# Performance work log

Measured on AMD Instinct MI355X. Metric: run time of the kernel, lower is better.

Reference implementation:

```python
import jax, jax.numpy as jnp
import numpy as np

N = 50000
D = 64
E = 800000


def setup_inputs() -> dict:
    key = jax.random.key(0)
    ks = jax.random.split(key, 8)
    x = jax.random.normal(ks[0], (N, D), dtype=jnp.float32)
    edge_index = jax.random.randint(ks[1], (2, E), 0, N, dtype=jnp.int64)
    edge_attr = jax.random.normal(ks[2], (E,), dtype=jnp.float32)
    x_agg_emb = jax.random.normal(ks[3], (N, D), dtype=jnp.float32)
    # Linear(2D -> D) weights stored as [in, out]; scale ~ kaiming-ish
    W_msg = jax.random.normal(ks[4], (2 * D, D), dtype=jnp.float32) * (1.0 / np.sqrt(2 * D))
    b_msg = jnp.zeros((D,), dtype=jnp.float32)
    W_upd = jax.random.normal(ks[5], (2 * D, D), dtype=jnp.float32) * (1.0 / np.sqrt(2 * D))
    b_upd = jnp.zeros((D,), dtype=jnp.float32)
    return {"x": x, "edge_index": edge_index, "edge_attr": edge_attr,
            "x_agg_emb": x_agg_emb, "W_msg": W_msg, "b_msg": b_msg,
            "W_upd": W_upd, "b_upd": b_upd}


def reference(x, edge_index, edge_attr, x_agg_emb, W_msg, b_msg, W_upd, b_upd):
    col, row = edge_index[0], edge_index[1]
    # edge-weighted gather: [E, D]
    msgs = edge_attr[:, None] * x[col]
    # scatter-mean over destination nodes (dim_size = N)
    summed = jax.ops.segment_sum(msgs, row, num_segments=N)            # [N, D]
    counts = jax.ops.segment_sum(jnp.ones_like(edge_attr), row, num_segments=N)  # [N]
    x_agg = summed / jnp.maximum(counts, 1.0)[:, None]
    # message MLP: Linear(2D->D) + ReLU
    m = jax.nn.relu(jnp.concatenate([x_agg, x_agg_emb], axis=-1) @ W_msg + b_msg)
    # update MLP: Linear(2D->D) + ReLU
    out = jax.nn.relu(jnp.concatenate([x, m], axis=-1) @ W_upd + b_upd)
    return out
```

## Files before the change

### kernel.cpp

```cpp
#include <hip/hip_runtime.h>


#define CAP 64
#define FILLB 2048

typedef __attribute__((ext_vector_type(8))) short short8;
typedef __attribute__((ext_vector_type(4))) float f32x4;

__device__ __forceinline__ unsigned short f2bf(float f) {
    unsigned int u = __float_as_uint(f);
    u += 0x7FFFu + ((u >> 16) & 1u);
    return (unsigned short)(u >> 16);
}
__device__ __forceinline__ uint4 pack8(const float* v) {
    uint4 r;
    r.x = (unsigned)f2bf(v[0]) | ((unsigned)f2bf(v[1]) << 16);
    r.y = (unsigned)f2bf(v[2]) | ((unsigned)f2bf(v[3]) << 16);
    r.z = (unsigned)f2bf(v[4]) | ((unsigned)f2bf(v[5]) << 16);
    r.w = (unsigned)f2bf(v[6]) | ((unsigned)f2bf(v[7]) << 16);
    return r;
}

__global__ __launch_bounds__(256) void zero_f32(float* p, int n) {
    int i = blockIdx.x * 256 + threadIdx.x;
    if (i < n) p[i] = 0.0f;
}
__global__ __launch_bounds__(256) void zero_i32(int* p, int n) {
    int i = blockIdx.x * 256 + threadIdx.x;
    if (i < n) p[i] = 0;
}

__global__ __launch_bounds__(256) void fill_group_kernel(
    const int* __restrict__ ei, const float* __restrict__ ea,
    int* cnt, int2* __restrict__ packed, int E, int N)
{
    const int g   = blockIdx.x & 7;
    const int bg  = blockIdx.x >> 3;
    const int nb  = gridDim.x >> 3;
    const int rpg = (N + 7) >> 3;
    const int rlo = g * rpg;
    const int rhi = min(rlo + rpg, N);
    const int chunk = (E + nb - 1) / nb;
    const int lo = bg * chunk;
    const int hi = min(lo + chunk, E);
    for (int e = lo + (int)threadIdx.x; e < hi; e += 256) {
        int row = ei[E + e];
        if (row >= rlo && row < rhi) {
            int pos = atomicAdd(&cnt[row], 1);
            if (pos < CAP)
                packed[(size_t)row * CAP + pos] =
                    make_int2(ei[e], __float_as_int(ea[e]));
        }
    }
}

__global__ __launch_bounds__(256) void gather_cap_kernel(
    const int2* __restrict__ packed, const int* __restrict__ cnt,
    const float* __restrict__ x, float* __restrict__ out, int N)
{
    const int g   = blockIdx.x & 7;
    const int i   = blockIdx.x >> 3;
    const int rpg = (N + 7) >> 3;
    const int nlo = g * rpg;
    int n = nlo + i * 4 + ((int)threadIdx.x >> 6);
    if (n >= nlo + rpg || n >= N) return;
    int lane = threadIdx.x & 63;
    const int2* seg = packed + (size_t)n * CAP;
    int deg = cnt[n];
    int dl = min(deg, CAP);
    float a0 = 0.f, a1 = 0.f, a2 = 0.f, a3 = 0.f;
    int j = 0;
    for (; j + 4 <= dl; j += 4) {
        int4 q0 = ((const int4*)seg)[(j >> 1)];
        int4 q1 = ((const int4*)seg)[(j >> 1) + 1];
        a0 += __int_as_float(q0.y) * x[(size_t)q0.x * 64 + lane];
        a1 += __int_as_float(q0.w) * x[(size_t)q0.z * 64 + lane];
        a2 += __int_as_float(q1.y) * x[(size_t)q1.x * 64 + lane];
        a3 += __int_as_float(q1.w) * x[(size_t)q1.z * 64 + lane];
    }
    for (; j < dl; j++) {
        int2 p = seg[j];
        a0 += __int_as_float(p.y) * x[(size_t)p.x * 64 + lane];
    }
    float acc = (a0 + a1) + (a2 + a3);
    out[(size_t)n * 64 + lane] = acc / fmaxf((float)deg, 1.0f);
}


__global__ __launch_bounds__(256) void hist_kernel(
    const int* __restrict__ ei, int* hist, int E)
{
    int e = blockIdx.x * 256 + threadIdx.x;
    if (e < E) atomicAdd(&hist[ei[E + e]], 1);
}
__global__ __launch_bounds__(256) void scan_partial_kernel(
    const int* __restrict__ hist, int* partial, int N)
{
    __shared__ int s[256];
    int t = threadIdx.x;
    int i = blockIdx.x * 256 + t;
    s[t] = (i < N) ? hist[i] : 0;
    __syncthreads();
    #pragma unroll
    for (int off = 128; off > 0; off >>= 1) {
        if (t < off) s[t] += s[t + off];
        __syncthreads();
    }
    if (t == 0) partial[blockIdx.x] = s[0];
}
__global__ __launch_bounds__(256) void scan_top_kernel(
    const int* __restrict__ partial, int* scanP, int NB)
{
    __shared__ int s[256];
    int t = threadIdx.x;
    int v = (t < NB) ? partial[t] : 0;
    s[t] = v;
    __syncthreads();
    #pragma unroll
    for (int off = 1; off < 256; off <<= 1) {
        int add = (t >= off) ? s[t - off] : 0;
        __syncthreads();
        s[t] += add;
        __syncthreads();
    }
    if (t < NB) scanP[t] = s[t] - v;
}
__global__ __launch_bounds__(256) void scan_final_kernel(
    const int* __restrict__ hist, const int* __restrict__ scanP,
    int* offsets, int* cursor, int N)
{
    __shared__ int s[256];
    int t = threadIdx.x;
    int i = blockIdx.x * 256 + t;
    int v = (i < N) ? hist[i] : 0;
    s[t] = v;
    __syncthreads();
    #pragma unroll
    for (int off = 1; off < 256; off <<= 1) {
        int add = (t >= off) ? s[t - off] : 0;
        __syncthreads();
        s[t] += add;
        __syncthreads();
    }
    if (i < N) {
        int o = scanP[blockIdx.x] + s[t] - v;
        offsets[i] = o;
        cursor[i]  = o;
    }
}
__global__ __launch_bounds__(256) void fill_kernel(
    const int* __restrict__ ei, const float* __restrict__ ea,
    int* cursor, int2* __restrict__ packed, int E)
{
    int e = blockIdx.x * 256 + threadIdx.x;
    if (e >= E) return;
    int pos = atomicAdd(&cursor[ei[E + e]], 1);
    packed[pos] = make_int2(ei[e], __float_as_int(ea[e]));
}
__global__ __launch_bounds__(256) void gather_kernel(
    const int2* __restrict__ packed, const int* __restrict__ offsets,
    const int* __restrict__ hist, const float* __restrict__ x,
    float* __restrict__ out, int N)
{
    int t = threadIdx.x;
    int n = blockIdx.x * 4 + (t >> 6);
    int lane = t & 63;
    if (n >= N) return;
    int start = offsets[n];
    int deg   = hist[n];
    float a0 = 0.f, a1 = 0.f, a2 = 0.f, a3 = 0.f;
    int j = 0;
    for (; j + 4 <= deg; j += 4) {
        int2 p0 = packed[start + j];
        int2 p1 = packed[start + j + 1];
        int2 p2 = packed[start + j + 2];
        int2 p3 = packed[start + j + 3];
        a0 += __int_as_float(p0.y) * x[(size_t)p0.x * 64 + lane];
        a1 += __int_as_float(p1.y) * x[(size_t)p1.x * 64 + lane];
        a2 += __int_as_float(p2.y) * x[(size_t)p2.x * 64 + lane];
        a3 += __int_as_float(p3.y) * x[(size_t)p3.x * 64 + lane];
    }
    for (; j < deg; j++) {
        int2 p = packed[start + j];
        a0 += __int_as_float(p.y) * x[(size_t)p.x * 64 + lane];
    }
    float acc = (a0 + a1) + (a2 + a3);
    out[(size_t)n * 64 + lane] = acc / fmaxf((float)deg, 1.0f);
}


__global__ __launch_bounds__(256) void scatter_kernel(
    const int* __restrict__ ei, const float* __restrict__ ea,
    const float* __restrict__ x, float* summed, float* counts, int E)
{
    int idx = blockIdx.x * 256 + threadIdx.x;
    int e = idx >> 6;
    int d = idx & 63;
    if (e >= E) return;
    float v = ea[e] * x[(size_t)ei[e] * 64 + d];
    atomicAdd(&summed[(size_t)ei[E + e] * 64 + d], v);
    if (d == 0) atomicAdd(&counts[ei[E + e]], 1.0f);
}


__device__ __forceinline__ void stage_W(
    unsigned short* Wb, const float* Wg, int t)
{
    #pragma unroll
    for (int c = t; c < 1024; c += 256) {
        int R = c >> 6, nn = c & 63;
        int kt = R >> 2, qq = R & 3;
        const float* src = Wg + (size_t)(kt * 32 + qq * 8) * 64 + nn;
        float v[8];
        #pragma unroll
        for (int j = 0; j < 8; j++) v[j] = src[(size_t)j * 64];
        *(uint4*)&Wb[R * 528 + nn * 8] = pack8(v);
    }
}

__device__ __forceinline__ void mfma_tile(
    const unsigned short* Ab, const unsigned short* Wb,
    int wv, int lane, f32x4 acc[4])
{
    const int q  = lane >> 4;
    const int ln = lane & 15;
    const int rr = wv * 16 + ln;
    short8 af[4];
    #pragma unroll
    for (int kt = 0; kt < 4; kt++)
        af[kt] = *(const short8*)&Ab[rr * 128 + (((kt * 4 + q) ^ ln) * 8)];
    #pragma unroll
    for (int nt = 0; nt < 4; nt++) {
        #pragma unroll
        for (int kt = 0; kt < 4; kt++) {
            short8 bf = *(const short8*)&Wb[(kt * 4 + q) * 528 + (nt * 16 + ln) * 8];
            acc[nt] = __builtin_amdgcn_mfma_f32_16x16x32_bf16(af[kt], bf, acc[nt], 0, 0, 0);
        }
    }
}

__global__ __launch_bounds__(256) void mfma_mlp(
    const float* Aagg, const float* __restrict__ Aemb,
    const float* __restrict__ counts, const float* __restrict__ Xin,
    const float* __restrict__ Wm, const float* __restrict__ bm,
    const float* __restrict__ Wu, const float* __restrict__ bu,
    float* out, int N)
{
    __shared__ __align__(16) unsigned short Ab[64 * 128];
    __shared__ __align__(16) unsigned short Wb[16 * 528];

    const int t = threadIdx.x;
    const int tile0 = blockIdx.x * 64;
    const int lane = t & 63, wv = t >> 6;
    const int q = lane >> 4, ln = lane & 15;

    stage_W(Wb, Wm, t);
    #pragma unroll
    for (int s = t; s < 1024; s += 256) {
        int r = s >> 4, chunk = s & 15;
        int node = tile0 + r;
        float v[8] = {0.f, 0.f, 0.f, 0.f, 0.f, 0.f, 0.f, 0.f};
        if (node < N) {
            const float* src = (chunk < 8)
                ? (Aagg + (size_t)node * 64 + chunk * 8)
                : (Aemb + (size_t)node * 64 + (chunk - 8) * 8);
            float4 p0 = ((const float4*)src)[0];
            float4 p1 = ((const float4*)src)[1];
            v[0] = p0.x; v[1] = p0.y; v[2] = p0.z; v[3] = p0.w;
            v[4] = p1.x; v[5] = p1.y; v[6] = p1.z; v[7] = p1.w;
            if (counts && chunk < 8) {
                float rc = 1.0f / fmaxf(counts[node], 1.0f);
                #pragma unroll
                for (int i = 0; i < 8; i++) v[i] *= rc;
            }
        }
        *(uint4*)&Ab[r * 128 + ((chunk ^ (r & 15)) * 8)] = pack8(v);
    }
    __syncthreads();

    f32x4 acc[4];
    #pragma unroll
    for (int nt = 0; nt < 4; nt++) acc[nt] = (f32x4){0.f, 0.f, 0.f, 0.f};
    mfma_tile(Ab, Wb, wv, lane, acc);
    __syncthreads();

    stage_W(Wb, Wu, t);
    #pragma unroll
    for (int s = t; s < 512; s += 256) {
        int r = s >> 3, chunk = s & 7;
        int node = tile0 + r;
        float v[8] = {0.f, 0.f, 0.f, 0.f, 0.f, 0.f, 0.f, 0.f};
        if (node < N) {
            const float* src = Xin + (size_t)node * 64 + chunk * 8;
            float4 p0 = ((const float4*)src)[0];
            float4 p1 = ((const float4*)src)[1];
            v[0] = p0.x; v[1] = p0.y; v[2] = p0.z; v[3] = p0.w;
            v[4] = p1.x; v[5] = p1.y; v[6] = p1.z; v[7] = p1.w;
        }
        *(uint4*)&Ab[r * 128 + ((chunk ^ (r & 15)) * 8)] = pack8(v);
    }
    #pragma unroll
    for (int nt = 0; nt < 4; nt++) {
        float bmv = bm[nt * 16 + ln];
        #pragma unroll
        for (int reg = 0; reg < 4; reg++) {
            float mv = fmaxf(acc[nt][reg] + bmv, 0.f);
            int rr = wv * 16 + q * 4 + reg;
            int k  = 64 + nt * 16 + ln;
            int ch = k >> 3;
            Ab[rr * 128 + ((ch ^ (rr & 15)) * 8) + (k & 7)] = f2bf(mv);
        }
    }
    __syncthreads();

    f32x4 acc2[4];
    #pragma unroll
    for (int nt = 0; nt < 4; nt++) acc2[nt] = (f32x4){0.f, 0.f, 0.f, 0.f};
    mfma_tile(Ab, Wb, wv, lane, acc2);
    #pragma unroll
    for (int nt = 0; nt < 4; nt++) {
        float buv = bu[nt * 16 + ln];
        #pragma unroll
        for (int reg = 0; reg < 4; reg++) {
            int rr = wv * 16 + q * 4 + reg;
            int node = tile0 + rr;
            if (node < N)
                out[(size_t)node * 64 + nt * 16 + ln] =
                    fmaxf(acc2[nt][reg] + buv, 0.f);
        }
    }
}

extern "C" void kernel_launch(void* const* d_in, const int* in_sizes, int n_in,
                              void* d_out, int out_size, void* d_ws, size_t ws_size,
                              hipStream_t stream) {
    const float* x   = (const float*)d_in[0];
    const int*   ei  = (const int*)d_in[1];
    const float* ea  = (const float*)d_in[2];
    const float* emb = (const float*)d_in[3];
    const float* Wm  = (const float*)d_in[4];
    const float* bm  = (const float*)d_in[5];
    const float* Wu  = (const float*)d_in[6];
    const float* bu  = (const float*)d_in[7];
    float*       out = (float*)d_out;

    const int N = in_sizes[0] / 64;
    const int E = in_sizes[2];
    const int NB = (N + 255) / 256;

    const int eblocks = (E + 255) / 256;
    const int mblocks = (N + 63) / 64;
    const int rpg = (N + 7) / 8;

    const size_t need_cap = (size_t)N * CAP * 8 + (size_t)N * 4;
    const size_t need_csr = (size_t)E * 8 + ((size_t)3 * N + 512) * 4;

    if (ws_size >= need_cap) {
        char* ws = (char*)d_ws;
        int2* packed = (int2*)ws;
        int*  cnt    = (int*)(ws + (size_t)N * CAP * 8);

        zero_i32<<<NB, 256, 0, stream>>>(cnt, N);
        fill_group_kernel<<<FILLB, 256, 0, stream>>>(ei, ea, cnt, packed, E, N);
        int gblocks = 8 * ((rpg + 3) / 4);
        gather_cap_kernel<<<gblocks, 256, 0, stream>>>(packed, cnt, x, out, N);
        mfma_mlp<<<mblocks, 256, 0, stream>>>(out, emb, nullptr, x,
                                              Wm, bm, Wu, bu, out, N);
    } else if (ws_size >= need_csr && NB <= 256) {
        char* ws = (char*)d_ws;
        int2* packed  = (int2*)ws;
        int*  hist    = (int*)(ws + (size_t)E * 8);
        int*  offsets = hist + N;
        int*  cursor  = offsets + N;
        int*  partial = cursor + N;
        int*  scanP   = partial + 256;

        zero_i32<<<NB, 256, 0, stream>>>(hist, N);
        hist_kernel<<<eblocks, 256, 0, stream>>>(ei, hist, E);
        scan_partial_kernel<<<NB, 256, 0, stream>>>(hist, partial, N);
        scan_top_kernel<<<1, 256, 0, stream>>>(partial, scanP, NB);
        scan_final_kernel<<<NB, 256, 0, stream>>>(hist, scanP, offsets, cursor, N);
        fill_kernel<<<eblocks, 256, 0, stream>>>(ei, ea, cursor, packed, E);
        gather_kernel<<<(N + 3) / 4, 256, 0, stream>>>(packed, offsets, hist, x, out, N);
        mfma_mlp<<<mblocks, 256, 0, stream>>>(out, emb, nullptr, x,
                                              Wm, bm, Wu, bu, out, N);
    } else {
        float* counts = (float*)d_ws;
        zero_f32<<<(N * 64 + 255) / 256, 256, 0, stream>>>(out, N * 64);
        zero_f32<<<NB, 256, 0, stream>>>(counts, N);
        long long total = (long long)E * 64;
        scatter_kernel<<<(int)((total + 255) / 256), 256, 0, stream>>>(
            ei, ea, x, out, counts, E);
        mfma_mlp<<<mblocks, 256, 0, stream>>>(out, emb, counts, x,
                                              Wm, bm, Wu, bu, out, N);
    }
}
```

Baseline: 174.5 us.

## Convert node features to bf16 upfront and gather/MLP on bf16 buffers

Adds a prep kernel that converts x and x_agg_emb to bf16 once and also zeroes the degree counters, replacing the separate zero kernel. The gather then reads bf16 rows of x and writes a bf16 aggregate, and a new MLP kernel loads bf16 tiles straight into shared memory without converting them. This halves the bytes moved by the random-access gather and by the MLP loads. In exchange it adds an extra pass over x and emb and extra workspace, and x is rounded to bf16 before aggregation, which changes numerics slightly.

```diff
diff --git a/kernel.cpp b/kernel.cpp
--- a/kernel.cpp
+++ b/kernel.cpp
@@ -11,6 +11,9 @@
     unsigned int u = __float_as_uint(f);
     u += 0x7FFFu + ((u >> 16) & 1u);
     return (unsigned short)(u >> 16);
+}
+__device__ __forceinline__ float bf2f(unsigned short u) {
+    return __uint_as_float((unsigned int)u << 16);
 }
 __device__ __forceinline__ uint4 pack8(const float* v) {
     uint4 r;
@@ -28,6 +31,29 @@
 __global__ __launch_bounds__(256) void zero_i32(int* p, int n) {
     int i = blockIdx.x * 256 + threadIdx.x;
     if (i < n) p[i] = 0;
+}
+
+__global__ __launch_bounds__(256) void prep_kernel(
+    const float* __restrict__ x, const float* __restrict__ emb,
+    unsigned short* __restrict__ xb, unsigned short* __restrict__ eb,
+    int* __restrict__ cnt, int N)
+{
+    int i = blockIdx.x * 256 + threadIdx.x;
+    int base = i * 8;
+    if (base < N * 64) {
+        float v[8];
+        float4 p0 = ((const float4*)(x + base))[0];
+        float4 p1 = ((const float4*)(x + base))[1];
+        v[0]=p0.x; v[1]=p0.y; v[2]=p0.z; v[3]=p0.w;
+        v[4]=p1.x; v[5]=p1.y; v[6]=p1.z; v[7]=p1.w;
+        *(uint4*)(xb + base) = pack8(v);
+        p0 = ((const float4*)(emb + base))[0];
+        p1 = ((const float4*)(emb + base))[1];
+        v[0]=p0.x; v[1]=p0.y; v[2]=p0.z; v[3]=p0.w;
+        v[4]=p1.x; v[5]=p1.y; v[6]=p1.z; v[7]=p1.w;
+        *(uint4*)(eb + base) = pack8(v);
+    }
+    if (i < N) cnt[i] = 0;
 }
 
 __global__ __launch_bounds__(256) void fill_group_kernel(
@@ -54,9 +80,10 @@
     }
 }
 
-__global__ __launch_bounds__(256) void gather_cap_kernel(
+__global__ __launch_bounds__(256) void gather_bf_kernel(
     const int2* __restrict__ packed, const int* __restrict__ cnt,
-    const float* __restrict__ x, float* __restrict__ out, int N)
+    const unsigned short* __restrict__ xb,
+    unsigned short* __restrict__ aggb, int N)
 {
     const int g   = blockIdx.x & 7;
     const int i   = blockIdx.x >> 3;
@@ -73,17 +100,17 @@
     for (; j + 4 <= dl; j += 4) {
         int4 q0 = ((const int4*)seg)[(j >> 1)];
         int4 q1 = ((const int4*)seg)[(j >> 1) + 1];
-        a0 += __int_as_float(q0.y) * x[(size_t)q0.x * 64 + lane];
-        a1 += __int_as_float(q0.w) * x[(size_t)q0.z * 64 + lane];
-        a2 += __int_as_float(q1.y) * x[(size_t)q1.x * 64 + lane];
-        a3 += __int_as_float(q1.w) * x[(size_t)q1.z * 64 + lane];
+        a0 += __int_as_float(q0.y) * bf2f(xb[(size_t)q0.x * 64 + lane]);
+        a1 += __int_as_float(q0.w) * bf2f(xb[(size_t)q0.z * 64 + lane]);
+        a2 += __int_as_float(q1.y) * bf2f(xb[(size_t)q1.x * 64 + lane]);
+        a3 += __int_as_float(q1.w) * bf2f(xb[(size_t)q1.z * 64 + lane]);
     }
     for (; j < dl; j++) {
         int2 p = seg[j];
-        a0 += __int_as_float(p.y) * x[(size_t)p.x * 64 + lane];
+        a0 += __int_as_float(p.y) * bf2f(xb[(size_t)p.x * 64 + lane]);
     }
     float acc = (a0 + a1) + (a2 + a3);
-    out[(size_t)n * 64 + lane] = acc / fmaxf((float)deg, 1.0f);
+    aggb[(size_t)n * 64 + lane] = f2bf(acc / fmaxf((float)deg, 1.0f));
 }
 
 
@@ -239,6 +266,84 @@
     }
 }
 
+__global__ __launch_bounds__(256) void mfma_mlp_bf(
+    const unsigned short* __restrict__ aggb, const unsigned short* __restrict__ eb,
+    const unsigned short* __restrict__ xb,
+    const float* __restrict__ Wm, const float* __restrict__ bm,
+    const float* __restrict__ Wu, const float* __restrict__ bu,
+    float* __restrict__ out, int N)
+{
+    __shared__ __align__(16) unsigned short Ab[64 * 128];
+    __shared__ __align__(16) unsigned short Wb[16 * 528];
+
+    const int t = threadIdx.x;
+    const int tile0 = blockIdx.x * 64;
+    const int lane = t & 63, wv = t >> 6;
+    const int q = lane >> 4, ln = lane & 15;
+
+    stage_W(Wb, Wm, t);
+    #pragma unroll
+    for (int s = t; s < 1024; s += 256) {
+        int r = s >> 4, chunk = s & 15;
+        int node = tile0 + r;
+        uint4 v = make_uint4(0u, 0u, 0u, 0u);
+        if (node < N) {
+            const unsigned short* src = (chunk < 8)
+                ? (aggb + (size_t)node * 64 + chunk * 8)
+                : (eb   + (size_t)node * 64 + (chunk - 8) * 8);
+            v = *(const uint4*)src;
+        }
+        *(uint4*)&Ab[r * 128 + ((chunk ^ (r & 15)) * 8)] = v;
+    }
+    __syncthreads();
+
+    f32x4 acc[4];
+    #pragma unroll
+    for (int nt = 0; nt < 4; nt++) acc[nt] = (f32x4){0.f, 0.f, 0.f, 0.f};
+    mfma_tile(Ab, Wb, wv, lane, acc);
+    __syncthreads();
+
+    stage_W(Wb, Wu, t);
+    #pragma unroll
+    for (int s = t; s < 512; s += 256) {
+        int r = s >> 3, chunk = s & 7;
+        int node = tile0 + r;
+        uint4 v = make_uint4(0u, 0u, 0u, 0u);
+        if (node < N) v = *(const uint4*)(xb + (size_t)node * 64 + chunk * 8);
+        *(uint4*)&Ab[r * 128 + ((chunk ^ (r & 15)) * 8)] = v;
+    }
+    #pragma unroll
+    for (int nt = 0; nt < 4; nt++) {
+        float bmv = bm[nt * 16 + ln];
+        #pragma unroll
+        for (int reg = 0; reg < 4; reg++) {
+            float mv = fmaxf(acc[nt][reg] + bmv, 0.f);
+            int rr = wv * 16 + q * 4 + reg;
+            int k  = 64 + nt * 16 + ln;
+            int ch = k >> 3;
+            Ab[rr * 128 + ((ch ^ (rr & 15)) * 8) + (k & 7)] = f2bf(mv);
+        }
+    }
+    __syncthreads();
+
+    f32x4 acc2[4];
+    #pragma unroll
+    for (int nt = 0; nt < 4; nt++) acc2[nt] = (f32x4){0.f, 0.f, 0.f, 0.f};
+    mfma_tile(Ab, Wb, wv, lane, acc2);
+    #pragma unroll
+    for (int nt = 0; nt < 4; nt++) {
+        float buv = bu[nt * 16 + ln];
+        #pragma unroll
+        for (int reg = 0; reg < 4; reg++) {
+            int rr = wv * 16 + q * 4 + reg;
+            int node = tile0 + rr;
+            if (node < N)
+                out[(size_t)node * 64 + nt * 16 + ln] =
+                    fmaxf(acc2[nt][reg] + buv, 0.f);
+        }
+    }
+}
+
 __global__ __launch_bounds__(256) void mfma_mlp(
     const float* Aagg, const float* __restrict__ Aemb,
     const float* __restrict__ counts, const float* __restrict__ Xin,
@@ -266,8 +371,8 @@
                 : (Aemb + (size_t)node * 64 + (chunk - 8) * 8);
             float4 p0 = ((const float4*)src)[0];
             float4 p1 = ((const float4*)src)[1];
-            v[0] = p0.x; v[1] = p0.y; v[2] = p0.z; v[3] = p0.w;
-            v[4] = p1.x; v[5] = p1.y; v[6] = p1.z; v[7] = p1.w;
+            v[0]=p0.x; v[1]=p0.y; v[2]=p0.z; v[3]=p0.w;
+            v[4]=p1.x; v[5]=p1.y; v[6]=p1.z; v[7]=p1.w;
             if (counts && chunk < 8) {
                 float rc = 1.0f / fmaxf(counts[node], 1.0f);
                 #pragma unroll
@@ -294,8 +399,8 @@
             const float* src = Xin + (size_t)node * 64 + chunk * 8;
             float4 p0 = ((const float4*)src)[0];
             float4 p1 = ((const float4*)src)[1];
-            v[0] = p0.x; v[1] = p0.y; v[2] = p0.z; v[3] = p0.w;
-            v[4] = p1.x; v[5] = p1.y; v[6] = p1.z; v[7] = p1.w;
+            v[0]=p0.x; v[1]=p0.y; v[2]=p0.z; v[3]=p0.w;
+            v[4]=p1.x; v[5]=p1.y; v[6]=p1.z; v[7]=p1.w;
         }
         *(uint4*)&Ab[r * 128 + ((chunk ^ (r & 15)) * 8)] = pack8(v);
     }
@@ -352,20 +457,24 @@
     const int mblocks = (N + 63) / 64;
     const int rpg = (N + 7) / 8;
 
-    const size_t need_cap = (size_t)N * CAP * 8 + (size_t)N * 4;
+    const size_t packed_b = (size_t)N * CAP * 8;
+    const size_t need_bf  = packed_b + (size_t)N * 4 + (size_t)3 * N * 128;
     const size_t need_csr = (size_t)E * 8 + ((size_t)3 * N + 512) * 4;
 
-    if (ws_size >= need_cap) {
+    if (ws_size >= need_bf) {
         char* ws = (char*)d_ws;
-        int2* packed = (int2*)ws;
-        int*  cnt    = (int*)(ws + (size_t)N * CAP * 8);
-
-        zero_i32<<<NB, 256, 0, stream>>>(cnt, N);
+        int2*           packed = (int2*)ws;
+        int*            cnt    = (int*)(ws + packed_b);
+        unsigned short* xb     = (unsigned short*)(ws + packed_b + (size_t)N * 4);
+        unsigned short* eb     = xb + (size_t)N * 64;
+        unsigned short* aggb   = eb + (size_t)N * 64;
+
+        prep_kernel<<<(N * 8 + 255) / 256, 256, 0, stream>>>(x, emb, xb, eb, cnt, N);
         fill_group_kernel<<<FILLB, 256, 0, stream>>>(ei, ea, cnt, packed, E, N);
         int gblocks = 8 * ((rpg + 3) / 4);
-        gather_cap_kernel<<<gblocks, 256, 0, stream>>>(packed, cnt, x, out, N);
-        mfma_mlp<<<mblocks, 256, 0, stream>>>(out, emb, nullptr, x,
-                                              Wm, bm, Wu, bu, out, N);
+        gather_bf_kernel<<<gblocks, 256, 0, stream>>>(packed, cnt, xb, aggb, N);
+        mfma_mlp_bf<<<mblocks, 256, 0, stream>>>(aggb, eb, xb,
+                                                 Wm, bm, Wu, bu, out, N);
     } else if (ws_size >= need_csr && NB <= 256) {
         char* ws = (char*)d_ws;
         int2* packed  = (int2*)ws;
```

Result: slower. 178.2 us (+2.1%).
